# Optimization experiments

Hardware: AMD Instinct MI355X
Metric: run time of the kernel (lower is better)

The kernel has to match this reference:

```python
import jax, jax.numpy as jnp
import numpy as np

N_NODES = 50000
D_IN = 256
D_OUT = 128
N_POS = 1600000   # positive edges used for GCN aggregation
N_PRED = 500000   # edges to score


def setup_inputs() -> dict:
    key = jax.random.key(0)
    ks = jax.random.split(key, 6)
    x = jax.random.normal(ks[0], (N_NODES, D_IN), dtype=jnp.float32)
    pos_edge_index = jax.random.randint(ks[1], (2, N_POS), 0, N_NODES)
    edge_index = jax.random.randint(ks[2], (2, N_PRED), 0, N_NODES)
    # init_linear: Linear(d_in, d_in); stored as (in, out) so fwd is x @ W1 + b1
    W1 = jax.random.normal(ks[3], (D_IN, D_IN), dtype=jnp.float32) / np.sqrt(D_IN).astype(np.float32)
    b1 = jnp.zeros((D_IN,), dtype=jnp.float32)
    # GCNConv weight (in, out) and bias
    Wc = jax.random.normal(ks[4], (D_IN, D_OUT), dtype=jnp.float32) / np.sqrt(D_IN).astype(np.float32)
    bc = jnp.zeros((D_OUT,), dtype=jnp.float32)
    return dict(x=x, edge_index=edge_index, pos_edge_index=pos_edge_index,
                W1=W1, b1=b1, Wc=Wc, bc=bc)


def reference(x, edge_index, pos_edge_index, W1, b1, Wc, bc):
    n = x.shape[0]
    # init_linear
    h = x @ W1 + b1                                  # [N, D_IN]
    # GCNConv: linear transform first, then normalized scatter-add aggregation
    h = h @ Wc                                       # [N, D_OUT]
    # add self-loops (PyG GCNConv default add_self_loops=True, edge_weight=1)
    loops = jnp.arange(n, dtype=pos_edge_index.dtype)
    row = jnp.concatenate([pos_edge_index[0], loops])  # source
    col = jnp.concatenate([pos_edge_index[1], loops])  # target (aggregation)
    # symmetric normalization: deg over target, norm = d^-1/2[row]*d^-1/2[col]
    deg = jax.ops.segment_sum(jnp.ones_like(col, dtype=h.dtype), col, num_segments=n)
    dinv = jnp.where(deg > 0, jax.lax.rsqrt(deg), 0.0)
    norm = dinv[row] * dinv[col]                     # [E+N]
    msgs = h[row] * norm[:, None]                    # gather + scale
    out = jax.ops.segment_sum(msgs, col, num_segments=n) + bc  # scatter-add + bias
    # edge dot-product scoring
    logits = (out[edge_index[0]] * out[edge_index[1]]).sum(axis=-1)  # [N_PRED]
    return logits
```

## Files before the change

### kernel.cpp

```cpp
#include <hip/hip_runtime.h>

#define N_NODES 50000
#define D_IN 256
#define D_OUT 128
#define N_POS 1600000
#define N_PRED 500000

#define G_BUCKETS 782
#define GPAD 1024
#define SB 640
#define CHUNK 2500
#define CAP 4096
#define GEMM_BLOCKS 782
#define QPRED 125000

#define NT 4
#define TSZ 12500
#define NPB 32
#define AGGB 1563

typedef __attribute__((ext_vector_type(8))) short short8;
typedef __attribute__((ext_vector_type(4))) float f32x4;

__device__ __forceinline__ unsigned short f2bf(float f) {
    unsigned int u = __float_as_uint(f);
    u += 0x7FFFu + ((u >> 16) & 1u);
    return (unsigned short)(u >> 16);
}
__device__ __forceinline__ unsigned int pk2(float a, float b) {
    unsigned int ua = __float_as_uint(a), ub = __float_as_uint(b);
    ua += 0x7FFFu + ((ua >> 16) & 1u);
    ub += 0x7FFFu + ((ub >> 16) & 1u);
    return (ua >> 16) | (ub & 0xFFFF0000u);
}
__device__ __forceinline__ float bflo(unsigned int u) { return __uint_as_float(u << 16); }
__device__ __forceinline__ float bfhi(unsigned int u) { return __uint_as_float(u & 0xFFFF0000u); }

__device__ __forceinline__ float dot8(uint4 ua, uint4 ub) {
    return bflo(ua.x) * bflo(ub.x) + bfhi(ua.x) * bfhi(ub.x)
         + bflo(ua.y) * bflo(ub.y) + bfhi(ua.y) * bfhi(ub.y)
         + bflo(ua.z) * bflo(ub.z) + bfhi(ua.z) * bfhi(ub.z)
         + bflo(ua.w) * bflo(ub.w) + bfhi(ua.w) * bfhi(ub.w);
}

__global__ __launch_bounds__(256) void scatter_fuse_k(const int* __restrict__ row,
                                                      const int* __restrict__ col,
                                                      unsigned int* __restrict__ seg,
                                                      unsigned int* __restrict__ ebs,
                                                      const float* __restrict__ W1,
                                                      const float* __restrict__ Wc,
                                                      const float* __restrict__ b1,
                                                      unsigned short* __restrict__ Bp,
                                                      float* __restrict__ bf) {
    __shared__ __align__(16) char smem[23424];
    if (blockIdx.x < SB) {
        int* hist  = (int*)smem;
        int* lofs  = hist + GPAD;
        int* fill2 = lofs + GPAD;
        int* part  = fill2 + GPAD;
        unsigned int* stag = (unsigned int*)(part + 256);
        int t = threadIdx.x;
        int b = blockIdx.x;
        for (int i = t; i < GPAD; i += 256) { hist[i] = 0; fill2[i] = 0; }
        __syncthreads();
        int e0 = b * CHUNK;
        for (int i = t; i < CHUNK; i += 256)
            atomicAdd(&hist[col[e0 + i] >> 6], 1);
        __syncthreads();
        int h[4], p4 = 0;
        #pragma unroll
        for (int i = 0; i < 4; ++i) { h[i] = hist[4 * t + i]; p4 += h[i]; }
        part[t] = p4;
        __syncthreads();
        for (int d = 1; d < 256; d <<= 1) {
            int add = (t >= d) ? part[t - d] : 0;
            __syncthreads();
            part[t] += add;
            __syncthreads();
        }
        int ex = part[t] - p4;
        #pragma unroll
        for (int i = 0; i < 4; ++i) { lofs[4 * t + i] = ex; ex += h[i]; }
        __syncthreads();
        for (int g = t; g < G_BUCKETS; g += 256)
            seg[(long)g * SB + b] = (unsigned int)lofs[g] | ((unsigned int)hist[g] << 16);
        for (int i = t; i < CHUNK; i += 256) {
            int c = col[e0 + i];
            int g = c >> 6;
            unsigned int u = (unsigned int)row[e0 + i] | ((unsigned int)(c & 63) << 16);
            int lp = atomicAdd(&fill2[g], 1);
            stag[lofs[g] + lp] = u;
        }
        __syncthreads();
        for (int i = t; i < CHUNK; i += 256)
            ebs[(long)b * CHUNK + i] = stag[i];
    } else {
        int gid = (blockIdx.x - SB) * 256 + threadIdx.x;
        int k = gid >> 7;
        int n = gid & 127;
        float acc = 0.f;
        #pragma unroll 4
        for (int kk = 0; kk < D_IN; ++kk)
            acc += W1[k * D_IN + kk] * Wc[kk * D_OUT + n];
        int ks = k >> 5, q = (k >> 3) & 3, jj = k & 7;
        int nt = n >> 4, nl = n & 15;
        int lane = q * 16 + nl;
        Bp[(((long)(ks * 8 + nt)) * 64 + lane) * 8 + jj] = f2bf(acc);
        if (gid < D_OUT) {
            float accb = 0.f;
            for (int kk = 0; kk < D_IN; ++kk)
                accb += b1[kk] * Wc[kk * D_OUT + gid];
            bf[gid] = accb;
        }
    }
}

__global__ __launch_bounds__(256) void gemm_k(const float* __restrict__ x,
                                              const uint4* __restrict__ Bp,
                                              const float* __restrict__ bf,
                                              unsigned short* __restrict__ hsb) {
    __shared__ __align__(16) char smem[16384];
    const int wave = threadIdx.x >> 6;
    const int lane = threadIdx.x & 63;
    const int q    = lane >> 4;
    const int ml   = lane & 15;
    const int m0   = blockIdx.x * 64 + wave * 16;

    f32x4 acc[8];
    #pragma unroll
    for (int t = 0; t < 8; ++t) acc[t] = (f32x4){0.f, 0.f, 0.f, 0.f};

    long arow = m0 + ml; if (arow > N_NODES - 1) arow = N_NODES - 1;
    const float* xrow = x + arow * D_IN + q * 8;

    #pragma unroll
    for (int ks = 0; ks < 8; ++ks) {
        float4 xa = *(const float4*)(xrow + ks * 32);
        float4 xb = *(const float4*)(xrow + ks * 32 + 4);
        union { short8 s; unsigned int u[4]; } af;
        af.u[0] = pk2(xa.x, xa.y);
        af.u[1] = pk2(xa.z, xa.w);
        af.u[2] = pk2(xb.x, xb.y);
        af.u[3] = pk2(xb.z, xb.w);
        #pragma unroll
        for (int nt = 0; nt < 8; ++nt) {
            union { uint4 v; short8 s; } bu;
            bu.v = Bp[(long)(ks * 8 + nt) * 64 + lane];
            acc[nt] = __builtin_amdgcn_mfma_f32_16x16x32_bf16(af.s, bu.s, acc[nt], 0, 0, 0);
        }
    }

    unsigned short* o = (unsigned short*)smem + wave * 2048;
    #pragma unroll
    for (int nt = 0; nt < 8; ++nt) {
        float bn = bf[nt * 16 + ml];
        #pragma unroll
        for (int r = 0; r < 4; ++r) {
            float val = acc[nt][r] + bn;
            o[(q * 4 + r) * 128 + nt * 16 + ml] = f2bf(val);
        }
    }
    __syncthreads();
    #pragma unroll
    for (int i = 0; i < 4; ++i) {
        int fb = i * 1024 + lane * 16;
        int v = m0 + (fb >> 8);
        if (v < N_NODES) {
            uint4 val = *(const uint4*)((const char*)o + fb);
            *(uint4*)((char*)hsb + (long)v * 256 + (fb & 255)) = val;
        }
    }
}

__global__ __launch_bounds__(256) void csr_build_k(const unsigned int* __restrict__ seg,
                                                   const unsigned int* __restrict__ ebs,
                                                   unsigned short* __restrict__ csr,
                                                   int* __restrict__ offs5,
                                                   float* __restrict__ dinv,
                                                   uint4* __restrict__ hsb4) {
    __shared__ unsigned int stag[CAP];
    __shared__ unsigned short stag2[CAP];
    __shared__ int hist[256], lofs[256], fill[256], part[256];
    __shared__ float dloc[64];
    __shared__ int scnt;
    int t = threadIdx.x;
    int g = blockIdx.x;
    int s = g * CAP;
    hist[t] = 0; fill[t] = 0;
    const unsigned int* sg = seg + (long)g * SB;
    unsigned int w0 = sg[t];
    unsigned int w1 = sg[t + 256];
    unsigned int w2 = (t + 512 < SB) ? sg[t + 512] : 0u;
    int c0 = w0 >> 16, c1 = w1 >> 16, c2 = w2 >> 16;
    int lsum = c0 + c1 + c2;
    part[t] = lsum;
    __syncthreads();
    for (int d = 1; d < 256; d <<= 1) {
        int add = (t >= d) ? part[t - d] : 0;
        __syncthreads();
        part[t] += add;
        __syncthreads();
    }
    if (t == 255) scnt = part[255];
    int p = part[t] - lsum;
    {
        const unsigned int* e0p = ebs + (long)t * CHUNK + (w0 & 0xFFFFu);
        for (int k = 0; k < c0; ++k) stag[p + k] = e0p[k];
        p += c0;
        const unsigned int* e1p = ebs + (long)(t + 256) * CHUNK + (w1 & 0xFFFFu);
        for (int k = 0; k < c1; ++k) stag[p + k] = e1p[k];
        p += c1;
        const unsigned int* e2p = ebs + (long)(t + 512) * CHUNK + (w2 & 0xFFFFu);
        for (int k = 0; k < c2; ++k) stag[p + k] = e2p[k];
    }
    __syncthreads();
    int cnt = scnt;
    for (int i = t; i < cnt; i += 256) {
        unsigned int u = stag[i];
        int r = u & 0xFFFF;
        int tile = (r >= TSZ) + (r >= 2 * TSZ) + (r >= 3 * TSZ);
        atomicAdd(&hist[((u >> 16) & 63) * NT + tile], 1);
    }
    __syncthreads();
    int hv = hist[t];
    part[t] = hv;
    __syncthreads();
    for (int d = 1; d < 256; d <<= 1) {
        int add = (t >= d) ? part[t - d] : 0;
        __syncthreads();
        part[t] += add;
        __syncthreads();
    }
    lofs[t] = part[t] - hv;
    __syncthreads();
    if (t < 64) {
        int v = g * 64 + t;
        int b4 = t * NT;
        int cc0 = hist[b4], cc1 = hist[b4 + 1], cc2 = hist[b4 + 2], cc3 = hist[b4 + 3];
        float dl = rsqrtf((float)(cc0 + cc1 + cc2 + cc3) + 1.0f);
        dloc[t] = dl;
        if (v < N_NODES) {
            int o0 = s + lofs[b4];
            offs5[v * 5 + 0] = o0;
            offs5[v * 5 + 1] = o0 + cc0;
            offs5[v * 5 + 2] = o0 + cc0 + cc1;
            offs5[v * 5 + 3] = o0 + cc0 + cc1 + cc2;
            offs5[v * 5 + 4] = o0 + cc0 + cc1 + cc2 + cc3;
            dinv[v] = dl;
        }
    }
    for (int i = t; i < cnt; i += 256) {
        unsigned int u = stag[i];
        int r = u & 0xFFFF;
        int tile = (r >= TSZ) + (r >= 2 * TSZ) + (r >= 3 * TSZ);
        int key = ((u >> 16) & 63) * NT + tile;
        int lp = atomicAdd(&fill[key], 1);
        stag2[lofs[key] + lp] = (unsigned short)r;
    }
    __syncthreads();
    for (int i = t; i < cnt; i += 256)
        csr[s + i] = stag2[i];
    const int vb = g * 64;
    for (int i = t; i < 64 * 16; i += 256) {
        int n = i >> 4;
        int v = vb + n;
        if (v < N_NODES) {
            float d = dloc[n];
            long idx = (long)v * 16 + (i & 15);
            uint4 u = hsb4[idx];
            uint4 o;
            o.x = pk2(d * bflo(u.x), d * bfhi(u.x));
            o.y = pk2(d * bflo(u.y), d * bfhi(u.y));
            o.z = pk2(d * bflo(u.z), d * bfhi(u.z));
            o.w = pk2(d * bflo(u.w), d * bfhi(u.w));
            hsb4[idx] = o;
        }
    }
}

__global__ __launch_bounds__(256, 8) void aggregate_csr_k(const int* __restrict__ offs5,
                                                          const unsigned short* __restrict__ csr,
                                                          const uint4* __restrict__ hs4,
                                                          const float* __restrict__ dinv,
                                                          const float* __restrict__ bc,
                                                          uint4* __restrict__ feat4) {
    int tid = threadIdx.x;
    int li  = tid & 15;
    int g16 = tid >> 4;
    int v0 = blockIdx.x * NPB + g16 * 2;
    int v1 = v0 + 1;
    bool ok0 = v0 < N_NODES, ok1 = v1 < N_NODES;

    float a0[8] = {0.f, 0.f, 0.f, 0.f, 0.f, 0.f, 0.f, 0.f};
    float a1[8] = {0.f, 0.f, 0.f, 0.f, 0.f, 0.f, 0.f, 0.f};

    #pragma unroll 1
    for (int tt = 0; tt < NT; ++tt) {
        if (ok0) {
            int i  = offs5[v0 * 5 + tt];
            int s1 = offs5[v0 * 5 + tt + 1];
            for (; i + 3 < s1; i += 4) {
                int r0 = csr[i], r1 = csr[i + 1], r2 = csr[i + 2], r3 = csr[i + 3];
                uint4 u0 = hs4[r0 * 16 + li];
                uint4 u1 = hs4[r1 * 16 + li];
                uint4 u2 = hs4[r2 * 16 + li];
                uint4 u3 = hs4[r3 * 16 + li];
                __builtin_amdgcn_sched_barrier(0);
                a0[0] += (bflo(u0.x) + bflo(u1.x)) + (bflo(u2.x) + bflo(u3.x));
                a0[1] += (bfhi(u0.x) + bfhi(u1.x)) + (bfhi(u2.x) + bfhi(u3.x));
                a0[2] += (bflo(u0.y) + bflo(u1.y)) + (bflo(u2.y) + bflo(u3.y));
                a0[3] += (bfhi(u0.y) + bfhi(u1.y)) + (bfhi(u2.y) + bfhi(u3.y));
                a0[4] += (bflo(u0.z) + bflo(u1.z)) + (bflo(u2.z) + bflo(u3.z));
                a0[5] += (bfhi(u0.z) + bfhi(u1.z)) + (bfhi(u2.z) + bfhi(u3.z));
                a0[6] += (bflo(u0.w) + bflo(u1.w)) + (bflo(u2.w) + bflo(u3.w));
                a0[7] += (bfhi(u0.w) + bfhi(u1.w)) + (bfhi(u2.w) + bfhi(u3.w));
            }
            for (; i < s1; ++i) {
                int r = csr[i];
                uint4 u = hs4[r * 16 + li];
                a0[0] += bflo(u.x); a0[1] += bfhi(u.x);
                a0[2] += bflo(u.y); a0[3] += bfhi(u.y);
                a0[4] += bflo(u.z); a0[5] += bfhi(u.z);
                a0[6] += bflo(u.w); a0[7] += bfhi(u.w);
            }
        }
        if (ok1) {
            int i  = offs5[v1 * 5 + tt];
            int s1 = offs5[v1 * 5 + tt + 1];
            for (; i + 3 < s1; i += 4) {
                int r0 = csr[i], r1 = csr[i + 1], r2 = csr[i + 2], r3 = csr[i + 3];
                uint4 u0 = hs4[r0 * 16 + li];
                uint4 u1 = hs4[r1 * 16 + li];
                uint4 u2 = hs4[r2 * 16 + li];
                uint4 u3 = hs4[r3 * 16 + li];
                __builtin_amdgcn_sched_barrier(0);
                a1[0] += (bflo(u0.x) + bflo(u1.x)) + (bflo(u2.x) + bflo(u3.x));
                a1[1] += (bfhi(u0.x) + bfhi(u1.x)) + (bfhi(u2.x) + bfhi(u3.x));
                a1[2] += (bflo(u0.y) + bflo(u1.y)) + (bflo(u2.y) + bflo(u3.y));
                a1[3] += (bfhi(u0.y) + bfhi(u1.y)) + (bfhi(u2.y) + bfhi(u3.y));
                a1[4] += (bflo(u0.z) + bflo(u1.z)) + (bflo(u2.z) + bflo(u3.z));
                a1[5] += (bfhi(u0.z) + bfhi(u1.z)) + (bfhi(u2.z) + bfhi(u3.z));
                a1[6] += (bflo(u0.w) + bflo(u1.w)) + (bflo(u2.w) + bflo(u3.w));
                a1[7] += (bfhi(u0.w) + bfhi(u1.w)) + (bfhi(u2.w) + bfhi(u3.w));
            }
            for (; i < s1; ++i) {
                int r = csr[i];
                uint4 u = hs4[r * 16 + li];
                a1[0] += bflo(u.x); a1[1] += bfhi(u.x);
                a1[2] += bflo(u.y); a1[3] += bfhi(u.y);
                a1[4] += bflo(u.z); a1[5] += bfhi(u.z);
                a1[6] += bflo(u.w); a1[7] += bfhi(u.w);
            }
        }
    }
    float4 b0 = *(const float4*)(bc + li * 8);
    float4 b1 = *(const float4*)(bc + li * 8 + 4);
    if (ok0) {
        uint4 su = hs4[(long)v0 * 16 + li];
        float dv = dinv[v0];
        float f0 = dv * (a0[0] + bflo(su.x)) + b0.x;
        float f1 = dv * (a0[1] + bfhi(su.x)) + b0.y;
        float f2 = dv * (a0[2] + bflo(su.y)) + b0.z;
        float f3 = dv * (a0[3] + bfhi(su.y)) + b0.w;
        float f4 = dv * (a0[4] + bflo(su.z)) + b1.x;
        float f5 = dv * (a0[5] + bfhi(su.z)) + b1.y;
        float f6 = dv * (a0[6] + bflo(su.w)) + b1.z;
        float f7 = dv * (a0[7] + bfhi(su.w)) + b1.w;
        uint4 o;
        o.x = pk2(f0, f1); o.y = pk2(f2, f3); o.z = pk2(f4, f5); o.w = pk2(f6, f7);
        feat4[(long)v0 * 16 + li] = o;
    }
    if (ok1) {
        uint4 su = hs4[(long)v1 * 16 + li];
        float dv = dinv[v1];
        float f0 = dv * (a1[0] + bflo(su.x)) + b0.x;
        float f1 = dv * (a1[1] + bfhi(su.x)) + b0.y;
        float f2 = dv * (a1[2] + bflo(su.y)) + b0.z;
        float f3 = dv * (a1[3] + bfhi(su.y)) + b0.w;
        float f4 = dv * (a1[4] + bflo(su.z)) + b1.x;
        float f5 = dv * (a1[5] + bfhi(su.z)) + b1.y;
        float f6 = dv * (a1[6] + bflo(su.w)) + b1.z;
        float f7 = dv * (a1[7] + bfhi(su.w)) + b1.w;
        uint4 o;
        o.x = pk2(f0, f1); o.y = pk2(f2, f3); o.z = pk2(f4, f5); o.w = pk2(f6, f7);
        feat4[(long)v1 * 16 + li] = o;
    }
}

__global__ void score_k(const int* __restrict__ src, const int* __restrict__ dst,
                        const uint4* __restrict__ feat4, float* __restrict__ out) {
    int gid = blockIdx.x * blockDim.x + threadIdx.x;
    int e = gid >> 4;
    int c = gid & 15;
    if (e >= QPRED) return;
    int e0 = e, e1 = e + QPRED, e2 = e + 2 * QPRED, e3 = e + 3 * QPRED;
    int a0 = src[e0], b0 = dst[e0];
    int a1 = src[e1], b1 = dst[e1];
    int a2 = src[e2], b2 = dst[e2];
    int a3 = src[e3], b3 = dst[e3];
    uint4 ua0 = feat4[(long)a0 * 16 + c];
    uint4 ub0 = feat4[(long)b0 * 16 + c];
    uint4 ua1 = feat4[(long)a1 * 16 + c];
    uint4 ub1 = feat4[(long)b1 * 16 + c];
    uint4 ua2 = feat4[(long)a2 * 16 + c];
    uint4 ub2 = feat4[(long)b2 * 16 + c];
    uint4 ua3 = feat4[(long)a3 * 16 + c];
    uint4 ub3 = feat4[(long)b3 * 16 + c];
    float p0 = dot8(ua0, ub0);
    float p1 = dot8(ua1, ub1);
    float p2 = dot8(ua2, ub2);
    float p3 = dot8(ua3, ub3);
    #pragma unroll
    for (int m = 8; m; m >>= 1) {
        p0 += __shfl_xor(p0, m, 16);
        p1 += __shfl_xor(p1, m, 16);
        p2 += __shfl_xor(p2, m, 16);
        p3 += __shfl_xor(p3, m, 16);
    }
    if (c == 0) {
        out[e0] = p0;
        out[e1] = p1;
        out[e2] = p2;
        out[e3] = p3;
    }
}

extern "C" void kernel_launch(void* const* d_in, const int* in_sizes, int n_in,
                              void* d_out, int out_size, void* d_ws, size_t ws_size,
                              hipStream_t stream) {
    const float* x   = (const float*)d_in[0];
    const int*   ei  = (const int*)  d_in[1];
    const int*   pe  = (const int*)  d_in[2];
    const float* W1  = (const float*)d_in[3];
    const float* b1  = (const float*)d_in[4];
    const float* Wc  = (const float*)d_in[5];
    const float* bc  = (const float*)d_in[6];
    float* out = (float*)d_out;

    const int* pe_row = pe;
    const int* pe_col = pe + N_POS;
    const int* ei_src = ei;
    const int* ei_dst = ei + N_PRED;

    char* w = (char*)d_ws;
    unsigned short* Bp = (unsigned short*)w;  w += 32768 * 2;
    float* bf    = (float*)w;                 w += 128 * 4;
    float* dinv  = (float*)w;                 w += 50000 * 4;
    int*   offs5 = (int*)w;                   w += 50000 * 5 * 4;
    unsigned int* seg = (unsigned int*)w;     w += (long)G_BUCKETS * SB * 4;
    unsigned int* ebs = (unsigned int*)w;     w += (long)SB * CHUNK * 4;
    unsigned short* csr = (unsigned short*)w; w += (long)G_BUCKETS * CAP * 2;
    unsigned short* hsb   = (unsigned short*)w;  w += (long)N_NODES * D_OUT * 2;
    unsigned short* featb = (unsigned short*)w;

    scatter_fuse_k<<<SB + 128, 256, 0, stream>>>(pe_row, pe_col, seg, ebs,
                                                 W1, Wc, b1, Bp, bf);

    gemm_k        <<<GEMM_BLOCKS, 256, 0, stream>>>(x, (const uint4*)Bp, bf, hsb);

    csr_build_k   <<<G_BUCKETS, 256, 0, stream>>>(seg, ebs, csr, offs5, dinv,
                                                  (uint4*)hsb);

    aggregate_csr_k<<<AGGB, 256, 0, stream>>>(offs5, csr, (const uint4*)hsb,
                                              dinv, bc, (uint4*)featb);

    score_k       <<<(QPRED * 16 + 255) / 256, 256, 0, stream>>>(
                      ei_src, ei_dst, (const uint4*)featb, out);
}
```

Measured before the change: 232.1 us.

## Merge GEMM and CSR build into one launch, apply source dinv during aggregation

Combines the GEMM and CSR-build kernels into a single launch whose blocks branch on blockIdx, so the two independent stages run concurrently and one launch boundary disappears. The CSR build no longer pre-scales hsb by dinv in place, which saves a full read-modify-write pass over the hidden features. Instead, aggregation loads dinv[r] per neighbor and uses FMAs, and the self-loop term is scaled by dv. This trades extra per-edge dinv gathers in the aggregation loop for the removed pass, and drops the sched_barrier that was there before. Shared memory per block grows to the union of both stages' needs, which may lower occupancy for the GEMM blocks.

```diff
diff --git a/kernel.cpp b/kernel.cpp
--- a/kernel.cpp
+++ b/kernel.cpp
@@ -115,165 +115,150 @@
     }
 }
 
-__global__ __launch_bounds__(256) void gemm_k(const float* __restrict__ x,
-                                              const uint4* __restrict__ Bp,
-                                              const float* __restrict__ bf,
-                                              unsigned short* __restrict__ hsb) {
-    __shared__ __align__(16) char smem[16384];
-    const int wave = threadIdx.x >> 6;
-    const int lane = threadIdx.x & 63;
-    const int q    = lane >> 4;
-    const int ml   = lane & 15;
-    const int m0   = blockIdx.x * 64 + wave * 16;
-
-    f32x4 acc[8];
-    #pragma unroll
-    for (int t = 0; t < 8; ++t) acc[t] = (f32x4){0.f, 0.f, 0.f, 0.f};
-
-    long arow = m0 + ml; if (arow > N_NODES - 1) arow = N_NODES - 1;
-    const float* xrow = x + arow * D_IN + q * 8;
-
-    #pragma unroll
-    for (int ks = 0; ks < 8; ++ks) {
-        float4 xa = *(const float4*)(xrow + ks * 32);
-        float4 xb = *(const float4*)(xrow + ks * 32 + 4);
-        union { short8 s; unsigned int u[4]; } af;
-        af.u[0] = pk2(xa.x, xa.y);
-        af.u[1] = pk2(xa.z, xa.w);
-        af.u[2] = pk2(xb.x, xb.y);
-        af.u[3] = pk2(xb.z, xb.w);
+__global__ __launch_bounds__(256) void gemm_csr_k(const unsigned int* __restrict__ seg,
+                                                  const unsigned int* __restrict__ ebs,
+                                                  unsigned short* __restrict__ csr,
+                                                  int* __restrict__ offs5,
+                                                  float* __restrict__ dinv,
+                                                  const float* __restrict__ x,
+                                                  const uint4* __restrict__ Bp,
+                                                  const float* __restrict__ bf,
+                                                  unsigned short* __restrict__ hsb) {
+    __shared__ __align__(16) char smem[28704];
+    if (blockIdx.x < G_BUCKETS) {
+        unsigned int* stag = (unsigned int*)smem;
+        unsigned short* stag2 = (unsigned short*)(smem + 16384);
+        int* hist = (int*)(smem + 24576);
+        int* lofs = hist + 256;
+        int* fill = lofs + 256;
+        int* part = fill + 256;
+        __shared__ int scnt;
+        int t = threadIdx.x;
+        int g = blockIdx.x;
+        int s = g * CAP;
+        hist[t] = 0; fill[t] = 0;
+        const unsigned int* sg = seg + (long)g * SB;
+        unsigned int w0 = sg[t];
+        unsigned int w1 = sg[t + 256];
+        unsigned int w2 = (t + 512 < SB) ? sg[t + 512] : 0u;
+        int c0 = w0 >> 16, c1 = w1 >> 16, c2 = w2 >> 16;
+        int lsum = c0 + c1 + c2;
+        part[t] = lsum;
+        __syncthreads();
+        for (int d = 1; d < 256; d <<= 1) {
+            int add = (t >= d) ? part[t - d] : 0;
+            __syncthreads();
+            part[t] += add;
+            __syncthreads();
+        }
+        if (t == 255) scnt = part[255];
+        int p = part[t] - lsum;
+        {
+            const unsigned int* e0p = ebs + (long)t * CHUNK + (w0 & 0xFFFFu);
+            for (int k = 0; k < c0; ++k) stag[p + k] = e0p[k];
+            p += c0;
+            const unsigned int* e1p = ebs + (long)(t + 256) * CHUNK + (w1 & 0xFFFFu);
+            for (int k = 0; k < c1; ++k) stag[p + k] = e1p[k];
+            p += c1;
+            const unsigned int* e2p = ebs + (long)(t + 512) * CHUNK + (w2 & 0xFFFFu);
+            for (int k = 0; k < c2; ++k) stag[p + k] = e2p[k];
+        }
+        __syncthreads();
+        int cnt = scnt;
+        for (int i = t; i < cnt; i += 256) {
+            unsigned int u = stag[i];
+            int r = u & 0xFFFF;
+            int tile = (r >= TSZ) + (r >= 2 * TSZ) + (r >= 3 * TSZ);
+            atomicAdd(&hist[((u >> 16) & 63) * NT + tile], 1);
+        }
+        __syncthreads();
+        int hv = hist[t];
+        part[t] = hv;
+        __syncthreads();
+        for (int d = 1; d < 256; d <<= 1) {
+            int add = (t >= d) ? part[t - d] : 0;
+            __syncthreads();
+            part[t] += add;
+            __syncthreads();
+        }
+        lofs[t] = part[t] - hv;
+        __syncthreads();
+        if (t < 64) {
+            int v = g * 64 + t;
+            if (v < N_NODES) {
+                int b4 = t * NT;
+                int cc0 = hist[b4], cc1 = hist[b4 + 1], cc2 = hist[b4 + 2], cc3 = hist[b4 + 3];
+                int o0 = s + lofs[b4];
+                offs5[v * 5 + 0] = o0;
+                offs5[v * 5 + 1] = o0 + cc0;
+                offs5[v * 5 + 2] = o0 + cc0 + cc1;
+                offs5[v * 5 + 3] = o0 + cc0 + cc1 + cc2;
+                offs5[v * 5 + 4] = o0 + cc0 + cc1 + cc2 + cc3;
+                dinv[v] = rsqrtf((float)(cc0 + cc1 + cc2 + cc3) + 1.0f);
+            }
+        }
+        for (int i = t; i < cnt; i += 256) {
+            unsigned int u = stag[i];
+            int r = u & 0xFFFF;
+            int tile = (r >= TSZ) + (r >= 2 * TSZ) + (r >= 3 * TSZ);
+            int key = ((u >> 16) & 63) * NT + tile;
+            int lp = atomicAdd(&fill[key], 1);
+            stag2[lofs[key] + lp] = (unsigned short)r;
+        }
+        __syncthreads();
+        for (int i = t; i < cnt; i += 256)
+            csr[s + i] = stag2[i];
+    } else {
+        const int gb   = blockIdx.x - G_BUCKETS;
+        const int wave = threadIdx.x >> 6;
+        const int lane = threadIdx.x & 63;
+        const int q    = lane >> 4;
+        const int ml   = lane & 15;
+        const int m0   = gb * 64 + wave * 16;
+
+        f32x4 acc[8];
+        #pragma unroll
+        for (int t = 0; t < 8; ++t) acc[t] = (f32x4){0.f, 0.f, 0.f, 0.f};
+
+        long arow = m0 + ml; if (arow > N_NODES - 1) arow = N_NODES - 1;
+        const float* xrow = x + arow * D_IN + q * 8;
+
+        #pragma unroll
+        for (int ks = 0; ks < 8; ++ks) {
+            float4 xa = *(const float4*)(xrow + ks * 32);
+            float4 xb = *(const float4*)(xrow + ks * 32 + 4);
+            union { short8 s; unsigned int u[4]; } af;
+            af.u[0] = pk2(xa.x, xa.y);
+            af.u[1] = pk2(xa.z, xa.w);
+            af.u[2] = pk2(xb.x, xb.y);
+            af.u[3] = pk2(xb.z, xb.w);
+            #pragma unroll
+            for (int nt = 0; nt < 8; ++nt) {
+                union { uint4 v; short8 s; } bu;
+                bu.v = Bp[(long)(ks * 8 + nt) * 64 + lane];
+                acc[nt] = __builtin_amdgcn_mfma_f32_16x16x32_bf16(af.s, bu.s, acc[nt], 0, 0, 0);
+            }
+        }
+
+        unsigned short* o = (unsigned short*)smem + wave * 2048;
         #pragma unroll
         for (int nt = 0; nt < 8; ++nt) {
-            union { uint4 v; short8 s; } bu;
-            bu.v = Bp[(long)(ks * 8 + nt) * 64 + lane];
-            acc[nt] = __builtin_amdgcn_mfma_f32_16x16x32_bf16(af.s, bu.s, acc[nt], 0, 0, 0);
-        }
-    }
-
-    unsigned short* o = (unsigned short*)smem + wave * 2048;
-    #pragma unroll
-    for (int nt = 0; nt < 8; ++nt) {
-        float bn = bf[nt * 16 + ml];
-        #pragma unroll
-        for (int r = 0; r < 4; ++r) {
-            float val = acc[nt][r] + bn;
-            o[(q * 4 + r) * 128 + nt * 16 + ml] = f2bf(val);
-        }
-    }
-    __syncthreads();
-    #pragma unroll
-    for (int i = 0; i < 4; ++i) {
-        int fb = i * 1024 + lane * 16;
-        int v = m0 + (fb >> 8);
-        if (v < N_NODES) {
-            uint4 val = *(const uint4*)((const char*)o + fb);
-            *(uint4*)((char*)hsb + (long)v * 256 + (fb & 255)) = val;
-        }
-    }
-}
-
-__global__ __launch_bounds__(256) void csr_build_k(const unsigned int* __restrict__ seg,
-                                                   const unsigned int* __restrict__ ebs,
-                                                   unsigned short* __restrict__ csr,
-                                                   int* __restrict__ offs5,
-                                                   float* __restrict__ dinv,
-                                                   uint4* __restrict__ hsb4) {
-    __shared__ unsigned int stag[CAP];
-    __shared__ unsigned short stag2[CAP];
-    __shared__ int hist[256], lofs[256], fill[256], part[256];
-    __shared__ float dloc[64];
-    __shared__ int scnt;
-    int t = threadIdx.x;
-    int g = blockIdx.x;
-    int s = g * CAP;
-    hist[t] = 0; fill[t] = 0;
-    const unsigned int* sg = seg + (long)g * SB;
-    unsigned int w0 = sg[t];
-    unsigned int w1 = sg[t + 256];
-    unsigned int w2 = (t + 512 < SB) ? sg[t + 512] : 0u;
-    int c0 = w0 >> 16, c1 = w1 >> 16, c2 = w2 >> 16;
-    int lsum = c0 + c1 + c2;
-    part[t] = lsum;
-    __syncthreads();
-    for (int d = 1; d < 256; d <<= 1) {
-        int add = (t >= d) ? part[t - d] : 0;
-        __syncthreads();
-        part[t] += add;
-        __syncthreads();
-    }
-    if (t == 255) scnt = part[255];
-    int p = part[t] - lsum;
-    {
-        const unsigned int* e0p = ebs + (long)t * CHUNK + (w0 & 0xFFFFu);
-        for (int k = 0; k < c0; ++k) stag[p + k] = e0p[k];
-        p += c0;
-        const unsigned int* e1p = ebs + (long)(t + 256) * CHUNK + (w1 & 0xFFFFu);
-        for (int k = 0; k < c1; ++k) stag[p + k] = e1p[k];
-        p += c1;
-        const unsigned int* e2p = ebs + (long)(t + 512) * CHUNK + (w2 & 0xFFFFu);
-        for (int k = 0; k < c2; ++k) stag[p + k] = e2p[k];
-    }
-    __syncthreads();
-    int cnt = scnt;
-    for (int i = t; i < cnt; i += 256) {
-        unsigned int u = stag[i];
-        int r = u & 0xFFFF;
-        int tile = (r >= TSZ) + (r >= 2 * TSZ) + (r >= 3 * TSZ);
-        atomicAdd(&hist[((u >> 16) & 63) * NT + tile], 1);
-    }
-    __syncthreads();
-    int hv = hist[t];
-    part[t] = hv;
-    __syncthreads();
-    for (int d = 1; d < 256; d <<= 1) {
-        int add = (t >= d) ? part[t - d] : 0;
-        __syncthreads();
-        part[t] += add;
-        __syncthreads();
-    }
-    lofs[t] = part[t] - hv;
-    __syncthreads();
-    if (t < 64) {
-        int v = g * 64 + t;
-        int b4 = t * NT;
-        int cc0 = hist[b4], cc1 = hist[b4 + 1], cc2 = hist[b4 + 2], cc3 = hist[b4 + 3];
-        float dl = rsqrtf((float)(cc0 + cc1 + cc2 + cc3) + 1.0f);
-        dloc[t] = dl;
-        if (v < N_NODES) {
-            int o0 = s + lofs[b4];
-            offs5[v * 5 + 0] = o0;
-            offs5[v * 5 + 1] = o0 + cc0;
-            offs5[v * 5 + 2] = o0 + cc0 + cc1;
-            offs5[v * 5 + 3] = o0 + cc0 + cc1 + cc2;
-            offs5[v * 5 + 4] = o0 + cc0 + cc1 + cc2 + cc3;
-            dinv[v] = dl;
-        }
-    }
-    for (int i = t; i < cnt; i += 256) {
-        unsigned int u = stag[i];
-        int r = u & 0xFFFF;
-        int tile = (r >= TSZ) + (r >= 2 * TSZ) + (r >= 3 * TSZ);
-        int key = ((u >> 16) & 63) * NT + tile;
-        int lp = atomicAdd(&fill[key], 1);
-        stag2[lofs[key] + lp] = (unsigned short)r;
-    }
-    __syncthreads();
-    for (int i = t; i < cnt; i += 256)
-        csr[s + i] = stag2[i];
-    const int vb = g * 64;
-    for (int i = t; i < 64 * 16; i += 256) {
-        int n = i >> 4;
-        int v = vb + n;
-        if (v < N_NODES) {
-            float d = dloc[n];
-            long idx = (long)v * 16 + (i & 15);
-            uint4 u = hsb4[idx];
-            uint4 o;
-            o.x = pk2(d * bflo(u.x), d * bfhi(u.x));
-            o.y = pk2(d * bflo(u.y), d * bfhi(u.y));
-            o.z = pk2(d * bflo(u.z), d * bfhi(u.z));
-            o.w = pk2(d * bflo(u.w), d * bfhi(u.w));
-            hsb4[idx] = o;
+            float bn = bf[nt * 16 + ml];
+            #pragma unroll
+            for (int r = 0; r < 4; ++r) {
+                float val = acc[nt][r] + bn;
+                o[(q * 4 + r) * 128 + nt * 16 + ml] = f2bf(val);
+            }
+        }
+        __syncthreads();
+        #pragma unroll
+        for (int i = 0; i < 4; ++i) {
+            int fb = i * 1024 + lane * 16;
+            int v = m0 + (fb >> 8);
+            if (v < N_NODES) {
+                uint4 val = *(const uint4*)((const char*)o + fb);
+                *(uint4*)((char*)hsb + (long)v * 256 + (fb & 255)) = val;
+            }
         }
     }
 }
@@ -305,23 +290,32 @@
                 uint4 u1 = hs4[r1 * 16 + li];
                 uint4 u2 = hs4[r2 * 16 + li];
                 uint4 u3 = hs4[r3 * 16 + li];
-                __builtin_amdgcn_sched_barrier(0);
-                a0[0] += (bflo(u0.x) + bflo(u1.x)) + (bflo(u2.x) + bflo(u3.x));
-                a0[1] += (bfhi(u0.x) + bfhi(u1.x)) + (bfhi(u2.x) + bfhi(u3.x));
-                a0[2] += (bflo(u0.y) + bflo(u1.y)) + (bflo(u2.y) + bflo(u3.y));
-                a0[3] += (bfhi(u0.y) + bfhi(u1.y)) + (bfhi(u2.y) + bfhi(u3.y));
-                a0[4] += (bflo(u0.z) + bflo(u1.z)) + (bflo(u2.z) + bflo(u3.z));
-                a0[5] += (bfhi(u0.z) + bfhi(u1.z)) + (bfhi(u2.z) + bfhi(u3.z));
-                a0[6] += (bflo(u0.w) + bflo(u1.w)) + (bflo(u2.w) + bflo(u3.w));
-                a0[7] += (bfhi(u0.w) + bfhi(u1.w)) + (bfhi(u2.w) + bfhi(u3.w));
+                float d0 = dinv[r0], d1 = dinv[r1], d2 = dinv[r2], d3 = dinv[r3];
+                a0[0] = fmaf(d0, bflo(u0.x), a0[0]); a0[0] = fmaf(d1, bflo(u1.x), a0[0]);
+                a0[0] = fmaf(d2, bflo(u2.x), a0[0]); a0[0] = fmaf(d3, bflo(u3.x), a0[0]);
+                a0[1] = fmaf(d0, bfhi(u0.x), a0[1]); a0[1] = fmaf(d1, bfhi(u1.x), a0[1]);
+                a0[1] = fmaf(d2, bfhi(u2.x), a0[1]); a0[1] = fmaf(d3, bfhi(u3.x), a0[1]);
+                a0[2] = fmaf(d0, bflo(u0.y), a0[2]); a0[2] = fmaf(d1, bflo(u1.y), a0[2]);
+                a0[2] = fmaf(d2, bflo(u2.y), a0[2]); a0[2] = fmaf(d3, bflo(u3.y), a0[2]);
+                a0[3] = fmaf(d0, bfhi(u0.y), a0[3]); a0[3] = fmaf(d1, bfhi(u1.y), a0[3]);
+                a0[3] = fmaf(d2, bfhi(u2.y), a0[3]); a0[3] = fmaf(d3, bfhi(u3.y), a0[3]);
+                a0[4] = fmaf(d0, bflo(u0.z), a0[4]); a0[4] = fmaf(d1, bflo(u1.z), a0[4]);
+                a0[4] = fmaf(d2, bflo(u2.z), a0[4]); a0[4] = fmaf(d3, bflo(u3.z), a0[4]);
+                a0[5] = fmaf(d0, bfhi(u0.z), a0[5]); a0[5] = fmaf(d1, bfhi(u1.z), a0[5]);
+                a0[5] = fmaf(d2, bfhi(u2.z), a0[5]); a0[5] = fmaf(d3, bfhi(u3.z), a0[5]);
+                a0[6] = fmaf(d0, bflo(u0.w), a0[6]); a0[6] = fmaf(d1, bflo(u1.w), a0[6]);
+                a0[6] = fmaf(d2, bflo(u2.w), a0[6]); a0[6] = fmaf(d3, bflo(u3.w), a0[6]);
+                a0[7] = fmaf(d0, bfhi(u0.w), a0[7]); a0[7] = fmaf(d1, bfhi(u1.w), a0[7]);
+                a0[7] = fmaf(d2, bfhi(u2.w), a0[7]); a0[7] = fmaf(d3, bfhi(u3.w), a0[7]);
             }
             for (; i < s1; ++i) {
                 int r = csr[i];
                 uint4 u = hs4[r * 16 + li];
-                a0[0] += bflo(u.x); a0[1] += bfhi(u.x);
-                a0[2] += bflo(u.y); a0[3] += bfhi(u.y);
-                a0[4] += bflo(u.z); a0[5] += bfhi(u.z);
-                a0[6] += bflo(u.w); a0[7] += bfhi(u.w);
+                float d = dinv[r];
+                a0[0] = fmaf(d, bflo(u.x), a0[0]); a0[1] = fmaf(d, bfhi(u.x), a0[1]);
+                a0[2] = fmaf(d, bflo(u.y), a0[2]); a0[3] = fmaf(d, bfhi(u.y), a0[3]);
+                a0[4] = fmaf(d, bflo(u.z), a0[4]); a0[5] = fmaf(d, bfhi(u.z), a0[5]);
+                a0[6] = fmaf(d, bflo(u.w), a0[6]); a0[7] = fmaf(d, bfhi(u.w), a0[7]);
             }
         }
         if (ok1) {
@@ -333,23 +327,32 @@
                 uint4 u1 = hs4[r1 * 16 + li];
                 uint4 u2 = hs4[r2 * 16 + li];
                 uint4 u3 = hs4[r3 * 16 + li];
-                __builtin_amdgcn_sched_barrier(0);
-                a1[0] += (bflo(u0.x) + bflo(u1.x)) + (bflo(u2.x) + bflo(u3.x));
-                a1[1] += (bfhi(u0.x) + bfhi(u1.x)) + (bfhi(u2.x) + bfhi(u3.x));
-                a1[2] += (bflo(u0.y) + bflo(u1.y)) + (bflo(u2.y) + bflo(u3.y));
-                a1[3] += (bfhi(u0.y) + bfhi(u1.y)) + (bfhi(u2.y) + bfhi(u3.y));
-                a1[4] += (bflo(u0.z) + bflo(u1.z)) + (bflo(u2.z) + bflo(u3.z));
-                a1[5] += (bfhi(u0.z) + bfhi(u1.z)) + (bfhi(u2.z) + bfhi(u3.z));
-                a1[6] += (bflo(u0.w) + bflo(u1.w)) + (bflo(u2.w) + bflo(u3.w));
-                a1[7] += (bfhi(u0.w) + bfhi(u1.w)) + (bfhi(u2.w) + bfhi(u3.w));
+                float d0 = dinv[r0], d1 = dinv[r1], d2 = dinv[r2], d3 = dinv[r3];
+                a1[0] = fmaf(d0, bflo(u0.x), a1[0]); a1[0] = fmaf(d1, bflo(u1.x), a1[0]);
+                a1[0] = fmaf(d2, bflo(u2.x), a1[0]); a1[0] = fmaf(d3, bflo(u3.x), a1[0]);
+                a1[1] = fmaf(d0, bfhi(u0.x), a1[1]); a1[1] = fmaf(d1, bfhi(u1.x), a1[1]);
+                a1[1] = fmaf(d2, bfhi(u2.x), a1[1]); a1[1] = fmaf(d3, bfhi(u3.x), a1[1]);
+                a1[2] = fmaf(d0, bflo(u0.y), a1[2]); a1[2] = fmaf(d1, bflo(u1.y), a1[2]);
+                a1[2] = fmaf(d2, bflo(u2.y), a1[2]); a1[2] = fmaf(d3, bflo(u3.y), a1[2]);
+                a1[3] = fmaf(d0, bfhi(u0.y), a1[3]); a1[3] = fmaf(d1, bfhi(u1.y), a1[3]);
+                a1[3] = fmaf(d2, bfhi(u2.y), a1[3]); a1[3] = fmaf(d3, bfhi(u3.y), a1[3]);
+                a1[4] = fmaf(d0, bflo(u0.z), a1[4]); a1[4] = fmaf(d1, bflo(u1.z), a1[4]);
+                a1[4] = fmaf(d2, bflo(u2.z), a1[4]); a1[4] = fmaf(d3, bflo(u3.z), a1[4]);
+                a1[5] = fmaf(d0, bfhi(u0.z), a1[5]); a1[5] = fmaf(d1, bfhi(u1.z), a1[5]);
+                a1[5] = fmaf(d2, bfhi(u2.z), a1[5]); a1[5] = fmaf(d3, bfhi(u3.z), a1[5]);
+                a1[6] = fmaf(d0, bflo(u0.w), a1[6]); a1[6] = fmaf(d1, bflo(u1.w), a1[6]);
+                a1[6] = fmaf(d2, bflo(u2.w), a1[6]); a1[6] = fmaf(d3, bflo(u3.w), a1[6]);
+                a1[7] = fmaf(d0, bfhi(u0.w), a1[7]); a1[7] = fmaf(d1, bfhi(u1.w), a1[7]);
+                a1[7] = fmaf(d2, bfhi(u2.w), a1[7]); a1[7] = fmaf(d3, bfhi(u3.w), a1[7]);
             }
             for (; i < s1; ++i) {
                 int r = csr[i];
                 uint4 u = hs4[r * 16 + li];
-                a1[0] += bflo(u.x); a1[1] += bfhi(u.x);
-                a1[2] += bflo(u.y); a1[3] += bfhi(u.y);
-                a1[4] += bflo(u.z); a1[5] += bfhi(u.z);
-                a1[6] += bflo(u.w); a1[7] += bfhi(u.w);
+                float d = dinv[r];
+                a1[0] = fmaf(d, bflo(u.x), a1[0]); a1[1] = fmaf(d, bfhi(u.x), a1[1]);
+                a1[2] = fmaf(d, bflo(u.y), a1[2]); a1[3] = fmaf(d, bfhi(u.y), a1[3]);
+                a1[4] = fmaf(d, bflo(u.z), a1[4]); a1[5] = fmaf(d, bfhi(u.z), a1[5]);
+                a1[6] = fmaf(d, bflo(u.w), a1[6]); a1[7] = fmaf(d, bfhi(u.w), a1[7]);
             }
         }
     }
@@ -358,14 +361,14 @@
     if (ok0) {
         uint4 su = hs4[(long)v0 * 16 + li];
         float dv = dinv[v0];
-        float f0 = dv * (a0[0] + bflo(su.x)) + b0.x;
-        float f1 = dv * (a0[1] + bfhi(su.x)) + b0.y;
-        float f2 = dv * (a0[2] + bflo(su.y)) + b0.z;
-        float f3 = dv * (a0[3] + bfhi(su.y)) + b0.w;
-        float f4 = dv * (a0[4] + bflo(su.z)) + b1.x;
-        float f5 = dv * (a0[5] + bfhi(su.z)) + b1.y;
-        float f6 = dv * (a0[6] + bflo(su.w)) + b1.z;
-        float f7 = dv * (a0[7] + bfhi(su.w)) + b1.w;
+        float f0 = dv * (a0[0] + dv * bflo(su.x)) + b0.x;
+        float f1 = dv * (a0[1] + dv * bfhi(su.x)) + b0.y;
+        float f2 = dv * (a0[2] + dv * bflo(su.y)) + b0.z;
+        float f3 = dv * (a0[3] + dv * bfhi(su.y)) + b0.w;
+        float f4 = dv * (a0[4] + dv * bflo(su.z)) + b1.x;
+        float f5 = dv * (a0[5] + dv * bfhi(su.z)) + b1.y;
+        float f6 = dv * (a0[6] + dv * bflo(su.w)) + b1.z;
+        float f7 = dv * (a0[7] + dv * bfhi(su.w)) + b1.w;
         uint4 o;
         o.x = pk2(f0, f1); o.y = pk2(f2, f3); o.z = pk2(f4, f5); o.w = pk2(f6, f7);
         feat4[(long)v0 * 16 + li] = o;
@@ -373,14 +376,14 @@
     if (ok1) {
         uint4 su = hs4[(long)v1 * 16 + li];
         float dv = dinv[v1];
-        float f0 = dv * (a1[0] + bflo(su.x)) + b0.x;
-        float f1 = dv * (a1[1] + bfhi(su.x)) + b0.y;
-        float f2 = dv * (a1[2] + bflo(su.y)) + b0.z;
-        float f3 = dv * (a1[3] + bfhi(su.y)) + b0.w;
-        float f4 = dv * (a1[4] + bflo(su.z)) + b1.x;
-        float f5 = dv * (a1[5] + bfhi(su.z)) + b1.y;
-        float f6 = dv * (a1[6] + bflo(su.w)) + b1.z;
-        float f7 = dv * (a1[7] + bfhi(su.w)) + b1.w;
+        float f0 = dv * (a1[0] + dv * bflo(su.x)) + b0.x;
+        float f1 = dv * (a1[1] + dv * bfhi(su.x)) + b0.y;
+        float f2 = dv * (a1[2] + dv * bflo(su.y)) + b0.z;
+        float f3 = dv * (a1[3] + dv * bfhi(su.y)) + b0.w;
+        float f4 = dv * (a1[4] + dv * bflo(su.z)) + b1.x;
+        float f5 = dv * (a1[5] + dv * bfhi(su.z)) + b1.y;
+        float f6 = dv * (a1[6] + dv * bflo(su.w)) + b1.z;
+        float f7 = dv * (a1[7] + dv * bfhi(su.w)) + b1.w;
         uint4 o;
         o.x = pk2(f0, f1); o.y = pk2(f2, f3); o.z = pk2(f4, f5); o.w = pk2(f6, f7);
         feat4[(long)v1 * 16 + li] = o;
@@ -456,10 +459,9 @@
     scatter_fuse_k<<<SB + 128, 256, 0, stream>>>(pe_row, pe_col, seg, ebs,
                                                  W1, Wc, b1, Bp, bf);
 
-    gemm_k        <<<GEMM_BLOCKS, 256, 0, stream>>>(x, (const uint4*)Bp, bf, hsb);
-
-    csr_build_k   <<<G_BUCKETS, 256, 0, stream>>>(seg, ebs, csr, offs5, dinv,
-                                                  (uint4*)hsb);
+    gemm_csr_k    <<<G_BUCKETS + GEMM_BLOCKS, 256, 0, stream>>>(seg, ebs, csr, offs5,
+                                                                dinv, x, (const uint4*)Bp,
+                                                                bf, hsb);
 
     aggregate_csr_k<<<AGGB, 256, 0, stream>>>(offs5, csr, (const uint4*)hsb,
                                               dinv, bc, (uint4*)featb);
```

Result: no change. 230.8 us (-0.5%).

## Fuse GEMM and CSR build into one launch, computing degrees via global atomics

Applied to the files above, without the earlier changes.

Node degrees are now counted with global atomics during the scatter pass, so the GEMM epilogue can apply the d^-1/2 scaling directly. The GEMM and CSR-build kernels are merged into a single launch whose blocks split into two roles, so they run concurrently. This removes the extra read-modify-write pass over hsb that csr_build previously did. In exchange it adds a memset and 1.6M global atomics, and separately drops the sched_barrier in the aggregation loop.

```diff
diff --git a/kernel.cpp b/kernel.cpp
--- a/kernel.cpp
+++ b/kernel.cpp
@@ -47,6 +47,7 @@
                                                       const int* __restrict__ col,
                                                       unsigned int* __restrict__ seg,
                                                       unsigned int* __restrict__ ebs,
+                                                      int* __restrict__ deg,
                                                       const float* __restrict__ W1,
                                                       const float* __restrict__ Wc,
                                                       const float* __restrict__ b1,
@@ -64,8 +65,11 @@
         for (int i = t; i < GPAD; i += 256) { hist[i] = 0; fill2[i] = 0; }
         __syncthreads();
         int e0 = b * CHUNK;
-        for (int i = t; i < CHUNK; i += 256)
-            atomicAdd(&hist[col[e0 + i] >> 6], 1);
+        for (int i = t; i < CHUNK; i += 256) {
+            int c = col[e0 + i];
+            atomicAdd(&hist[c >> 6], 1);
+            atomicAdd(&deg[c], 1);
+        }
         __syncthreads();
         int h[4], p4 = 0;
         #pragma unroll
@@ -115,165 +119,160 @@
     }
 }
 
-__global__ __launch_bounds__(256) void gemm_k(const float* __restrict__ x,
-                                              const uint4* __restrict__ Bp,
-                                              const float* __restrict__ bf,
-                                              unsigned short* __restrict__ hsb) {
-    __shared__ __align__(16) char smem[16384];
-    const int wave = threadIdx.x >> 6;
-    const int lane = threadIdx.x & 63;
-    const int q    = lane >> 4;
-    const int ml   = lane & 15;
-    const int m0   = blockIdx.x * 64 + wave * 16;
-
-    f32x4 acc[8];
-    #pragma unroll
-    for (int t = 0; t < 8; ++t) acc[t] = (f32x4){0.f, 0.f, 0.f, 0.f};
-
-    long arow = m0 + ml; if (arow > N_NODES - 1) arow = N_NODES - 1;
-    const float* xrow = x + arow * D_IN + q * 8;
-
-    #pragma unroll
-    for (int ks = 0; ks < 8; ++ks) {
-        float4 xa = *(const float4*)(xrow + ks * 32);
-        float4 xb = *(const float4*)(xrow + ks * 32 + 4);
-        union { short8 s; unsigned int u[4]; } af;
-        af.u[0] = pk2(xa.x, xa.y);
-        af.u[1] = pk2(xa.z, xa.w);
-        af.u[2] = pk2(xb.x, xb.y);
-        af.u[3] = pk2(xb.z, xb.w);
+__global__ __launch_bounds__(256) void gemm_csr_k(const unsigned int* __restrict__ seg,
+                                                  const unsigned int* __restrict__ ebs,
+                                                  unsigned short* __restrict__ csr,
+                                                  int* __restrict__ offs5,
+                                                  const int* __restrict__ deg,
+                                                  float* __restrict__ dinv,
+                                                  const float* __restrict__ x,
+                                                  const uint4* __restrict__ Bp,
+                                                  const float* __restrict__ bf,
+                                                  unsigned short* __restrict__ hsb) {
+    __shared__ __align__(16) char smem[28704];
+    if (blockIdx.x < G_BUCKETS) {
+        unsigned int* stag = (unsigned int*)smem;
+        unsigned short* stag2 = (unsigned short*)(smem + 16384);
+        int* hist = (int*)(smem + 24576);
+        int* lofs = hist + 256;
+        int* fill = lofs + 256;
+        int* part = fill + 256;
+        __shared__ int scnt;
+        int t = threadIdx.x;
+        int g = blockIdx.x;
+        int s = g * CAP;
+        hist[t] = 0; fill[t] = 0;
+        const unsigned int* sg = seg + (long)g * SB;
+        unsigned int w0 = sg[t];
+        unsigned int w1 = sg[t + 256];
+        unsigned int w2 = (t + 512 < SB) ? sg[t + 512] : 0u;
+        int c0 = w0 >> 16, c1 = w1 >> 16, c2 = w2 >> 16;
+        int lsum = c0 + c1 + c2;
+        part[t] = lsum;
+        __syncthreads();
+        for (int d = 1; d < 256; d <<= 1) {
+            int add = (t >= d) ? part[t - d] : 0;
+            __syncthreads();
+            part[t] += add;
+            __syncthreads();
+        }
+        if (t == 255) scnt = part[255];
+        int p = part[t] - lsum;
+        {
+            const unsigned int* e0p = ebs + (long)t * CHUNK + (w0 & 0xFFFFu);
+            for (int k = 0; k < c0; ++k) stag[p + k] = e0p[k];
+            p += c0;
+            const unsigned int* e1p = ebs + (long)(t + 256) * CHUNK + (w1 & 0xFFFFu);
+            for (int k = 0; k < c1; ++k) stag[p + k] = e1p[k];
+            p += c1;
+            const unsigned int* e2p = ebs + (long)(t + 512) * CHUNK + (w2 & 0xFFFFu);
+            for (int k = 0; k < c2; ++k) stag[p + k] = e2p[k];
+        }
+        __syncthreads();
+        int cnt = scnt;
+        for (int i = t; i < cnt; i += 256) {
+            unsigned int u = stag[i];
+            int r = u & 0xFFFF;
+            int tile = (r >= TSZ) + (r >= 2 * TSZ) + (r >= 3 * TSZ);
+            atomicAdd(&hist[((u >> 16) & 63) * NT + tile], 1);
+        }
+        __syncthreads();
+        int hv = hist[t];
+        part[t] = hv;
+        __syncthreads();
+        for (int d = 1; d < 256; d <<= 1) {
+            int add = (t >= d) ? part[t - d] : 0;
+            __syncthreads();
+            part[t] += add;
+            __syncthreads();
+        }
+        lofs[t] = part[t] - hv;
+        __syncthreads();
+        if (t < 64) {
+            int v = g * 64 + t;
+            if (v < N_NODES) {
+                int b4 = t * NT;
+                int cc0 = hist[b4], cc1 = hist[b4 + 1], cc2 = hist[b4 + 2], cc3 = hist[b4 + 3];
+                int o0 = s + lofs[b4];
+                offs5[v * 5 + 0] = o0;
+                offs5[v * 5 + 1] = o0 + cc0;
+                offs5[v * 5 + 2] = o0 + cc0 + cc1;
+                offs5[v * 5 + 3] = o0 + cc0 + cc1 + cc2;
+                offs5[v * 5 + 4] = o0 + cc0 + cc1 + cc2 + cc3;
+            }
+        }
+        for (int i = t; i < cnt; i += 256) {
+            unsigned int u = stag[i];
+            int r = u & 0xFFFF;
+            int tile = (r >= TSZ) + (r >= 2 * TSZ) + (r >= 3 * TSZ);
+            int key = ((u >> 16) & 63) * NT + tile;
+            int lp = atomicAdd(&fill[key], 1);
+            stag2[lofs[key] + lp] = (unsigned short)r;
+        }
+        __syncthreads();
+        for (int i = t; i < cnt; i += 256)
+            csr[s + i] = stag2[i];
+    } else {
+        const int gb   = blockIdx.x - G_BUCKETS;
+        const int wave = threadIdx.x >> 6;
+        const int lane = threadIdx.x & 63;
+        const int q    = lane >> 4;
+        const int ml   = lane & 15;
+        const int m0   = gb * 64 + wave * 16;
+
+        if (threadIdx.x < 64) {
+            int v = gb * 64 + threadIdx.x;
+            if (v < N_NODES) dinv[v] = rsqrtf((float)deg[v] + 1.0f);
+        }
+
+        f32x4 acc[8];
+        #pragma unroll
+        for (int t = 0; t < 8; ++t) acc[t] = (f32x4){0.f, 0.f, 0.f, 0.f};
+
+        long arow = m0 + ml; if (arow > N_NODES - 1) arow = N_NODES - 1;
+        const float* xrow = x + arow * D_IN + q * 8;
+
+        #pragma unroll
+        for (int ks = 0; ks < 8; ++ks) {
+            float4 xa = *(const float4*)(xrow + ks * 32);
+            float4 xb = *(const float4*)(xrow + ks * 32 + 4);
+            union { short8 s; unsigned int u[4]; } af;
+            af.u[0] = pk2(xa.x, xa.y);
+            af.u[1] = pk2(xa.z, xa.w);
+            af.u[2] = pk2(xb.x, xb.y);
+            af.u[3] = pk2(xb.z, xb.w);
+            #pragma unroll
+            for (int nt = 0; nt < 8; ++nt) {
+                union { uint4 v; short8 s; } bu;
+                bu.v = Bp[(long)(ks * 8 + nt) * 64 + lane];
+                acc[nt] = __builtin_amdgcn_mfma_f32_16x16x32_bf16(af.s, bu.s, acc[nt], 0, 0, 0);
+            }
+        }
+
+        float dr[4];
+        #pragma unroll
+        for (int r = 0; r < 4; ++r)
+            dr[r] = rsqrtf((float)deg[m0 + q * 4 + r] + 1.0f);
+
+        unsigned short* o = (unsigned short*)smem + wave * 2048;
         #pragma unroll
         for (int nt = 0; nt < 8; ++nt) {
-            union { uint4 v; short8 s; } bu;
-            bu.v = Bp[(long)(ks * 8 + nt) * 64 + lane];
-            acc[nt] = __builtin_amdgcn_mfma_f32_16x16x32_bf16(af.s, bu.s, acc[nt], 0, 0, 0);
-        }
-    }
-
-    unsigned short* o = (unsigned short*)smem + wave * 2048;
-    #pragma unroll
-    for (int nt = 0; nt < 8; ++nt) {
-        float bn = bf[nt * 16 + ml];
-        #pragma unroll
-        for (int r = 0; r < 4; ++r) {
-            float val = acc[nt][r] + bn;
-            o[(q * 4 + r) * 128 + nt * 16 + ml] = f2bf(val);
-        }
-    }
-    __syncthreads();
-    #pragma unroll
-    for (int i = 0; i < 4; ++i) {
-        int fb = i * 1024 + lane * 16;
-        int v = m0 + (fb >> 8);
-        if (v < N_NODES) {
-            uint4 val = *(const uint4*)((const char*)o + fb);
-            *(uint4*)((char*)hsb + (long)v * 256 + (fb & 255)) = val;
-        }
-    }
-}
-
-__global__ __launch_bounds__(256) void csr_build_k(const unsigned int* __restrict__ seg,
-                                                   const unsigned int* __restrict__ ebs,
-                                                   unsigned short* __restrict__ csr,
-                                                   int* __restrict__ offs5,
-                                                   float* __restrict__ dinv,
-                                                   uint4* __restrict__ hsb4) {
-    __shared__ unsigned int stag[CAP];
-    __shared__ unsigned short stag2[CAP];
-    __shared__ int hist[256], lofs[256], fill[256], part[256];
-    __shared__ float dloc[64];
-    __shared__ int scnt;
-    int t = threadIdx.x;
-    int g = blockIdx.x;
-    int s = g * CAP;
-    hist[t] = 0; fill[t] = 0;
-    const unsigned int* sg = seg + (long)g * SB;
-    unsigned int w0 = sg[t];
-    unsigned int w1 = sg[t + 256];
-    unsigned int w2 = (t + 512 < SB) ? sg[t + 512] : 0u;
-    int c0 = w0 >> 16, c1 = w1 >> 16, c2 = w2 >> 16;
-    int lsum = c0 + c1 + c2;
-    part[t] = lsum;
-    __syncthreads();
-    for (int d = 1; d < 256; d <<= 1) {
-        int add = (t >= d) ? part[t - d] : 0;
-        __syncthreads();
-        part[t] += add;
-        __syncthreads();
-    }
-    if (t == 255) scnt = part[255];
-    int p = part[t] - lsum;
-    {
-        const unsigned int* e0p = ebs + (long)t * CHUNK + (w0 & 0xFFFFu);
-        for (int k = 0; k < c0; ++k) stag[p + k] = e0p[k];
-        p += c0;
-        const unsigned int* e1p = ebs + (long)(t + 256) * CHUNK + (w1 & 0xFFFFu);
-        for (int k = 0; k < c1; ++k) stag[p + k] = e1p[k];
-        p += c1;
-        const unsigned int* e2p = ebs + (long)(t + 512) * CHUNK + (w2 & 0xFFFFu);
-        for (int k = 0; k < c2; ++k) stag[p + k] = e2p[k];
-    }
-    __syncthreads();
-    int cnt = scnt;
-    for (int i = t; i < cnt; i += 256) {
-        unsigned int u = stag[i];
-        int r = u & 0xFFFF;
-        int tile = (r >= TSZ) + (r >= 2 * TSZ) + (r >= 3 * TSZ);
-        atomicAdd(&hist[((u >> 16) & 63) * NT + tile], 1);
-    }
-    __syncthreads();
-    int hv = hist[t];
-    part[t] = hv;
-    __syncthreads();
-    for (int d = 1; d < 256; d <<= 1) {
-        int add = (t >= d) ? part[t - d] : 0;
-        __syncthreads();
-        part[t] += add;
-        __syncthreads();
-    }
-    lofs[t] = part[t] - hv;
-    __syncthreads();
-    if (t < 64) {
-        int v = g * 64 + t;
-        int b4 = t * NT;
-        int cc0 = hist[b4], cc1 = hist[b4 + 1], cc2 = hist[b4 + 2], cc3 = hist[b4 + 3];
-        float dl = rsqrtf((float)(cc0 + cc1 + cc2 + cc3) + 1.0f);
-        dloc[t] = dl;
-        if (v < N_NODES) {
-            int o0 = s + lofs[b4];
-            offs5[v * 5 + 0] = o0;
-            offs5[v * 5 + 1] = o0 + cc0;
-            offs5[v * 5 + 2] = o0 + cc0 + cc1;
-            offs5[v * 5 + 3] = o0 + cc0 + cc1 + cc2;
-            offs5[v * 5 + 4] = o0 + cc0 + cc1 + cc2 + cc3;
-            dinv[v] = dl;
-        }
-    }
-    for (int i = t; i < cnt; i += 256) {
-        unsigned int u = stag[i];
-        int r = u & 0xFFFF;
-        int tile = (r >= TSZ) + (r >= 2 * TSZ) + (r >= 3 * TSZ);
-        int key = ((u >> 16) & 63) * NT + tile;
-        int lp = atomicAdd(&fill[key], 1);
-        stag2[lofs[key] + lp] = (unsigned short)r;
-    }
-    __syncthreads();
-    for (int i = t; i < cnt; i += 256)
-        csr[s + i] = stag2[i];
-    const int vb = g * 64;
-    for (int i = t; i < 64 * 16; i += 256) {
-        int n = i >> 4;
-        int v = vb + n;
-        if (v < N_NODES) {
-            float d = dloc[n];
-            long idx = (long)v * 16 + (i & 15);
-            uint4 u = hsb4[idx];
-            uint4 o;
-            o.x = pk2(d * bflo(u.x), d * bfhi(u.x));
-            o.y = pk2(d * bflo(u.y), d * bfhi(u.y));
-            o.z = pk2(d * bflo(u.z), d * bfhi(u.z));
-            o.w = pk2(d * bflo(u.w), d * bfhi(u.w));
-            hsb4[idx] = o;
+            float bn = bf[nt * 16 + ml];
+            #pragma unroll
+            for (int r = 0; r < 4; ++r) {
+                float val = (acc[nt][r] + bn) * dr[r];
+                o[(q * 4 + r) * 128 + nt * 16 + ml] = f2bf(val);
+            }
+        }
+        __syncthreads();
+        #pragma unroll
+        for (int i = 0; i < 4; ++i) {
+            int fb = i * 1024 + lane * 16;
+            int v = m0 + (fb >> 8);
+            if (v < N_NODES) {
+                uint4 val = *(const uint4*)((const char*)o + fb);
+                *(uint4*)((char*)hsb + (long)v * 256 + (fb & 255)) = val;
+            }
         }
     }
 }
@@ -305,7 +304,6 @@
                 uint4 u1 = hs4[r1 * 16 + li];
                 uint4 u2 = hs4[r2 * 16 + li];
                 uint4 u3 = hs4[r3 * 16 + li];
-                __builtin_amdgcn_sched_barrier(0);
                 a0[0] += (bflo(u0.x) + bflo(u1.x)) + (bflo(u2.x) + bflo(u3.x));
                 a0[1] += (bfhi(u0.x) + bfhi(u1.x)) + (bfhi(u2.x) + bfhi(u3.x));
                 a0[2] += (bflo(u0.y) + bflo(u1.y)) + (bflo(u2.y) + bflo(u3.y));
@@ -333,7 +331,6 @@
                 uint4 u1 = hs4[r1 * 16 + li];
                 uint4 u2 = hs4[r2 * 16 + li];
                 uint4 u3 = hs4[r3 * 16 + li];
-                __builtin_amdgcn_sched_barrier(0);
                 a1[0] += (bflo(u0.x) + bflo(u1.x)) + (bflo(u2.x) + bflo(u3.x));
                 a1[1] += (bfhi(u0.x) + bfhi(u1.x)) + (bfhi(u2.x) + bfhi(u3.x));
                 a1[2] += (bflo(u0.y) + bflo(u1.y)) + (bflo(u2.y) + bflo(u3.y));
@@ -446,6 +443,7 @@
     unsigned short* Bp = (unsigned short*)w;  w += 32768 * 2;
     float* bf    = (float*)w;                 w += 128 * 4;
     float* dinv  = (float*)w;                 w += 50000 * 4;
+    int*   deg   = (int*)w;                   w += 50048 * 4;
     int*   offs5 = (int*)w;                   w += 50000 * 5 * 4;
     unsigned int* seg = (unsigned int*)w;     w += (long)G_BUCKETS * SB * 4;
     unsigned int* ebs = (unsigned int*)w;     w += (long)SB * CHUNK * 4;
@@ -453,13 +451,14 @@
     unsigned short* hsb   = (unsigned short*)w;  w += (long)N_NODES * D_OUT * 2;
     unsigned short* featb = (unsigned short*)w;
 
-    scatter_fuse_k<<<SB + 128, 256, 0, stream>>>(pe_row, pe_col, seg, ebs,
+    hipMemsetAsync(deg, 0, 50048 * sizeof(int), stream);
+
+    scatter_fuse_k<<<SB + 128, 256, 0, stream>>>(pe_row, pe_col, seg, ebs, deg,
                                                  W1, Wc, b1, Bp, bf);
 
-    gemm_k        <<<GEMM_BLOCKS, 256, 0, stream>>>(x, (const uint4*)Bp, bf, hsb);
-
-    csr_build_k   <<<G_BUCKETS, 256, 0, stream>>>(seg, ebs, csr, offs5, dinv,
-                                                  (uint4*)hsb);
+    gemm_csr_k    <<<G_BUCKETS + GEMM_BLOCKS, 256, 0, stream>>>(seg, ebs, csr, offs5,
+                                                                deg, dinv, x,
+                                                                (const uint4*)Bp, bf, hsb);
 
     aggregate_csr_k<<<AGGB, 256, 0, stream>>>(offs5, csr, (const uint4*)hsb,
                                               dinv, bc, (uint4*)featb);
```

Result: slower. 280.1 us (+20.7%).
